# Kernel optimization log

Hardware: AMD Instinct MI355X
Metric: run time of the kernel (lower is better)

## Reference

```python
import jax, jax.numpy as jnp
import numpy as np

B = 16384    # number of paths (examples)
E = 100000   # num_entities
D = 256      # embedding_dim
H = 512      # hidden_dim = node_state_dim = msg_dim
T = 768      # text_dim
L = 2        # num_layers
R = 32       # num_relation_classes
EF = 8       # edge_feat_dim (hardcoded in module)
NUM_PROP = 2


def setup_inputs() -> dict:
    key = jax.random.key(0)
    ks = iter(jax.random.split(key, 40))
    def nrm(shape, s=0.02):
        return jax.random.normal(next(ks), shape, jnp.float32) * s
    z = lambda shape: jnp.zeros(shape, jnp.float32)
    inp = {
        "a_ids": jax.random.randint(next(ks), (B,), 0, E),
        "event_ids": jax.random.randint(next(ks), (B,), 0, E),
        "b_ids": jax.random.randint(next(ks), (B,), 0, E),
        "c_ids": jax.random.randint(next(ks), (B,), 0, E),
        "text_ab": jax.random.normal(next(ks), (B, T), jnp.float32),
        "ent_emb": nrm((E, D)),
        "text_W": nrm((T, D)), "text_b": z((D,)),
        "proj_W": nrm((D, H)), "proj_b": z((H,)),
        "msg_W1": nrm((L, H + EF, H)), "msg_b1": z((L, H)),
        "msg_W2": nrm((L, H, H)), "msg_b2": z((L, H)),
        "att_W1": nrm((L, H + EF, H // 2)), "att_b1": z((L, H // 2)),
        "att_W2": nrm((L, H // 2, H)), "att_b2": z((L, H)),
        "gru_Wih": nrm((L, 3 * H, H)), "gru_Whh": nrm((L, 3 * H, H)),
        "gru_bih": z((L, 3 * H)), "gru_bhh": z((L, 3 * H)),
        "head_W1": nrm((H, H)), "head_b1": z((H,)),
        "head_W2": nrm((H, R)), "head_b2": z((R,)),
    }
    return inp


def _forward(a_ids, event_ids, b_ids, c_ids, text_ab, ent_emb, text_W, text_b,
             proj_W, proj_b, msg_W1, msg_b1, msg_W2, msg_b2,
             att_W1, att_b1, att_W2, att_b2,
             gru_Wih, gru_Whh, gru_bih, gru_bhh,
             head_W1, head_b1, head_W2, head_b2):
    Bn = a_ids.shape[0]
    a_emb = ent_emb[a_ids]
    ev_emb = ent_emb[event_ids] + jax.nn.relu(text_ab @ text_W + text_b)  # text fused into Event node
    b_emb = ent_emb[b_ids]
    c_emb = ent_emb[c_ids]
    proj = lambda x: jax.nn.relu(x @ proj_W + proj_b)  # input_proj_ab (dropout=0 / eval)
    # merged graph: nodes [A(0:B), Event(B:2B), B(2B:3B), C(3B:4B)]
    state = jnp.concatenate([proj(a_emb), proj(ev_emb), proj(b_emb), proj(c_emb)], axis=0)  # [4B,H]
    ar = jnp.arange(Bn)
    src = jnp.concatenate([ar, ar + Bn, ar + Bn])             # A->Event, Event->B, Event->C
    dst = jnp.concatenate([ar + Bn, ar + 2 * Bn, ar + 3 * Bn])
    edge_feat = jax.nn.one_hot(jnp.repeat(jnp.arange(3), Bn), EF, dtype=state.dtype)  # [3B,8]
    n_layers = msg_W1.shape[0]
    for ii in range(n_layers):
        if ii > 0:
            state = jax.nn.relu(state)
        for _ in range(NUM_PROP):
            # gather node-pair diff + edge feature
            ein = jnp.concatenate([state[src] - state[dst], edge_feat], axis=1)  # [3B, H+EF]
            msg = jax.nn.relu(ein @ msg_W1[ii] + msg_b1[ii]) @ msg_W2[ii] + msg_b2[ii]
            att = jax.nn.sigmoid(jax.nn.relu(ein @ att_W1[ii] + att_b1[ii]) @ att_W2[ii] + att_b2[ii])
            agg = jax.ops.segment_sum(msg * att, dst, num_segments=4 * Bn)  # scatter_add
            # torch GRUCell update
            gi = agg @ gru_Wih[ii].T + gru_bih[ii]
            gh = state @ gru_Whh[ii].T + gru_bhh[ii]
            i_r, i_z, i_n = jnp.split(gi, 3, axis=-1)
            h_r, h_z, h_n = jnp.split(gh, 3, axis=-1)
            r = jax.nn.sigmoid(i_r + h_r)
            zg = jax.nn.sigmoid(i_z + h_z)
            n = jnp.tanh(i_n + r * h_n)
            state = (1.0 - zg) * n + zg * state
    # rel_AB predicted from node-state difference between A and B nodes
    diff = state[:Bn] - state[2 * Bn:3 * Bn]
    return jax.nn.relu(diff @ head_W1 + head_b1) @ head_W2 + head_b2  # [B, R] logits


def reference(a_ids, event_ids, b_ids, c_ids, text_ab, ent_emb, text_W, text_b,
              proj_W, proj_b, msg_W1, msg_b1, msg_W2, msg_b2,
              att_W1, att_b1, att_W2, att_b2,
              gru_Wih, gru_Whh, gru_bih, gru_bhh,
              head_W1, head_b1, head_W2, head_b2):
    return _forward(a_ids, event_ids, b_ids, c_ids, text_ab, ent_emb, text_W, text_b,
                    proj_W, proj_b, msg_W1, msg_b1, msg_W2, msg_b2,
                    att_W1, att_b1, att_W2, att_b2,
                    gru_Wih, gru_Whh, gru_bih, gru_bhh,
                    head_W1, head_b1, head_W2, head_b2)
```

## Files before the change

### kernel.cpp

```cpp
#include <hip/hip_runtime.h>
#include <math.h>


#define Bn 16384
#define Hn 512
#define Dn 256
#define Tn 768

#define EPI_NONE 0
#define EPI_RELU 1
#define EPI_SIG 2
#define EPI_SIGMUL 3
#define EPI_RELUGATHER 4
#define EPI_GRU 5

typedef unsigned short bfu;
typedef _Float16 f16;
typedef f16 h4 __attribute__((ext_vector_type(4)));
typedef f16 half8 __attribute__((ext_vector_type(8)));
typedef float floatx4 __attribute__((ext_vector_type(4)));

#define HTEXTW 0
#define HPROJW 196608
#define HHW1 327680
#define HWE1 589824
#define HMSGW2 1376256
#define HATTW2 1900544
#define HWIH 2162688
#define HWHH 3735552
#define HTOTAL 5308416
#define FTEXTB 0
#define FPROJB 256
#define FHB1 768
#define FGBIH 1280
#define FGBHH 4352
#define FBGRZ 7424
#define FBE1 9472
#define FBE2 14080

__device__ __forceinline__ float sigf(float x) { return 1.f / (1.f + expf(-x)); }

__device__ __forceinline__ float b2f(bfu v) {
  union { unsigned q; float f; } c;
  c.q = (unsigned)v << 16;
  return c.f;
}
__device__ __forceinline__ float4 bf4(uint2 u) {
  union { unsigned q; float f; } c;
  float4 r;
  c.q = u.x << 16;          r.x = c.f;
  c.q = u.x & 0xFFFF0000u;  r.y = c.f;
  c.q = u.y << 16;          r.z = c.f;
  c.q = u.y & 0xFFFF0000u;  r.w = c.f;
  return r;
}
__device__ __forceinline__ unsigned f2bu(float x) {
  union { float f; unsigned u; } c;
  c.f = x;
  return (c.u + 0x7FFFu + ((c.u >> 16) & 1u)) >> 16;
}
__device__ __forceinline__ float4 h2f4(h4 h) {
  return make_float4((float)h.x, (float)h.y, (float)h.z, (float)h.w);
}
__device__ __forceinline__ h4 f2h4c(float4 v) {
  h4 r;
  r.x = (f16)v.x; r.y = (f16)v.y; r.z = (f16)v.z; r.w = (f16)v.w;
  return r;
}
__device__ __forceinline__ half8 ff2h8(float4 a, float4 b) {
  half8 r;
  r[0] = (f16)a.x; r[1] = (f16)a.y; r[2] = (f16)a.z; r[3] = (f16)a.w;
  r[4] = (f16)b.x; r[5] = (f16)b.y; r[6] = (f16)b.z; r[7] = (f16)b.w;
  return r;
}
__device__ __forceinline__ half8 bf2h8(uint4 u) {
  uint2 lo; lo.x = u.x; lo.y = u.y;
  uint2 hi; hi.x = u.z; hi.y = u.w;
  return ff2h8(bf4(lo), bf4(hi));
}

__global__ void detect_k(const unsigned* __restrict__ p, int* __restrict__ flag) {
  __shared__ float red[256];
  const int t = threadIdx.x;
  union { unsigned q; float f; } c;
  c.q = p[t] << 16;
  float m = fabsf(c.f);
  if (!(m == m)) m = 1e30f;
  red[t] = m;
  __syncthreads();
  for (int s = 128; s > 0; s >>= 1) {
    if (t < s) red[t] = fmaxf(red[t], red[t + s]);
    __syncthreads();
  }
  if (t == 0) flag[0] = (red[0] < 1e3f) ? 1 : 0;
}

__device__ __forceinline__ float cvld(const void* p, size_t i, int fl) {
  return fl ? b2f(((const bfu*)p)[i]) : ((const float*)p)[i];
}

__global__ void convF_k(const void* __restrict__ src, size_t off, float* __restrict__ dst,
                        int n, const int* __restrict__ flagp) {
  const int i = blockIdx.x * 256 + threadIdx.x;
  if (i < n) dst[i] = cvld(src, off + i, flagp[0]);
}
__global__ void convH_k(const void* __restrict__ src, size_t off, f16* __restrict__ dst,
                        int n, const int* __restrict__ flagp) {
  const int i = blockIdx.x * 256 + threadIdx.x;
  if (i < n) dst[i] = (f16)cvld(src, off + i, flagp[0]);
}
__global__ void convT_k(const void* __restrict__ src, size_t off, f16* __restrict__ dst,
                        int K, int N, const int* __restrict__ flagp) {
  __shared__ f16 tile[32][33];
  const int t = threadIdx.x;
  const int c = t & 31, r0 = t >> 5;
  const int kb = blockIdx.y * 32, nb = blockIdx.x * 32;
  const int fl = flagp[0];
#pragma unroll
  for (int i = 0; i < 4; ++i)
    tile[r0 + i * 8][c] = (f16)cvld(src, off + (size_t)(kb + r0 + i * 8) * N + nb + c, fl);
  __syncthreads();
#pragma unroll
  for (int i = 0; i < 4; ++i)
    dst[(size_t)(nb + r0 + i * 8) * K + kb + c] = tile[c][r0 + i * 8];
}
__global__ void addv_k(const float* __restrict__ a, const float* __restrict__ b,
                       float* __restrict__ o, int n) {
  const int i = blockIdx.x * 256 + threadIdx.x;
  if (i < n) o[i] = a[i] + b[i];
}
__global__ void btype_k(const void* __restrict__ b, size_t bOff,
                        const void* __restrict__ wr, size_t wrOff,
                        float* __restrict__ dst, int N, int dstStride,
                        const int* __restrict__ flagp) {
  const int i = blockIdx.x * 256 + threadIdx.x;
  const int fl = flagp[0];
  if (i < 3 * N) {
    const int t = i / N, n = i % N;
    dst[(size_t)t * dstStride + n] = cvld(b, bOff + n, fl) + cvld(wr, wrOff + i, fl);
  }
}
__global__ void gather_k(const int* __restrict__ ids, const void* __restrict__ emb,
                         f16* __restrict__ Xc, const int* __restrict__ flagp) {
  const int r = blockIdx.x, t = threadIdx.x;
  const int id = ids[r];
  float4 v;
  if (flagp[0])
    v = bf4(((const uint2*)((const bfu*)emb + (size_t)id * Dn))[t]);
  else
    v = ((const float4*)((const float*)emb + (size_t)id * Dn))[t];
  ((h4*)(Xc + (size_t)r * Dn))[t] = f2h4c(v);
}

template <int EPI, int AM, int BM, int CT, int BTY>
__global__ __launch_bounds__(256, 2) void hgemm_k(
    const void* __restrict__ Ap, const void* __restrict__ Ap2,
    const f16* __restrict__ Wt, const f16* __restrict__ Wt2,
    const float* __restrict__ bias,
    const f16* __restrict__ ex1, const f16* __restrict__ ex2,
    const int* __restrict__ gidx, const void* __restrict__ gtab,
    void* __restrict__ C, int N, int K, int aStride, int rowOff, int nRows,
    const int* __restrict__ flagp) {
  __shared__ __align__(16) f16 As[128][40];
  __shared__ __align__(16) f16 Bs[128][40];
  const int t = threadIdx.x;
  const int bid = blockIdx.x;
  const int rowsPerX = nRows >> 3;
  const int slot = bid >> 3;
  const int row0 = ((bid & 7) * rowsPerX + slot % rowsPerX) * 128;
  const int col0 = (slot / rowsPerX) * 128;
  const int lane = t & 63;
  const int wv = t >> 6;
  const int wm = wv >> 1, wn = wv & 1;
  const int l16 = lane & 15, quad = lane >> 4;
  const int arow = t & 127;
  const int ak0 = (t >> 7) * 8;
  const int fl = (AM == 1 || EPI == EPI_RELUGATHER) ? flagp[0] : 0;

  floatx4 acc[4][4];
#pragma unroll
  for (int mi = 0; mi < 4; ++mi)
#pragma unroll
    for (int ni = 0; ni < 4; ++ni) acc[mi][ni] = (floatx4){0.f, 0.f, 0.f, 0.f};

  auto fetchA = [&](int kk, int seg) -> half8 {
    const int k = kk + ak0 + seg * 16;
    const int m = row0 + arow;
    if (AM == 5) {
      return *(const half8*)((const f16*)Ap + (size_t)m * aStride + k);
    } else if (AM == 1) {
      const size_t o = (size_t)(rowOff + m) * aStride + k;
      if (fl) return bf2h8(*(const uint4*)((const bfu*)Ap + o));
      const float* ap = (const float*)Ap + o;
      return ff2h8(*(const float4*)ap, *(const float4*)(ap + 4));
    } else if (AM == 6) {
      if (k < 512) return *(const half8*)((const f16*)Ap + (size_t)m * 512 + k);
      return *(const half8*)((const f16*)Ap2 + (size_t)m * 512 + (k - 512));
    } else {
      const int e = rowOff + m;
      const int s = (e < 2 * Bn) ? e : e - Bn;
      const f16* st = (const f16*)Ap;
      half8 x = *(const half8*)(st + (size_t)s * 512 + k);
      half8 y = *(const half8*)(st + (size_t)(e + Bn) * 512 + k);
      return x - y;
    }
  };
  auto fetchB = [&](int kk, int seg) -> half8 {
    const int k = kk + ak0 + seg * 16;
    const int n = col0 + arow;
    if (BM == 0) return *(const half8*)(Wt + (size_t)n * K + k);
    if (k < 512) return *(const half8*)(Wt + (size_t)n * 512 + k);
    return *(const half8*)(Wt2 + (size_t)n * 512 + k - 512);
  };

  half8 pa0 = fetchA(0, 0), pa1 = fetchA(0, 1);
  half8 pb0 = fetchB(0, 0), pb1 = fetchB(0, 1);

  int kt = 0;
  while (true) {
    __syncthreads();
    *(half8*)&As[arow][ak0] = pa0;
    *(half8*)&As[arow][ak0 + 16] = pa1;
    *(half8*)&Bs[arow][ak0] = pb0;
    *(half8*)&Bs[arow][ak0 + 16] = pb1;
    __syncthreads();
    const int kn = kt + 32;
    if (kn < K) {
      pa0 = fetchA(kn, 0); pa1 = fetchA(kn, 1);
      pb0 = fetchB(kn, 0); pb1 = fetchB(kn, 1);
    }
    half8 a8[4], b8[4];
#pragma unroll
    for (int mi = 0; mi < 4; ++mi)
      a8[mi] = *(const half8*)&As[wm * 64 + mi * 16 + l16][quad * 8];
#pragma unroll
    for (int ni = 0; ni < 4; ++ni)
      b8[ni] = *(const half8*)&Bs[wn * 64 + ni * 16 + l16][quad * 8];
#pragma unroll
    for (int mi = 0; mi < 4; ++mi)
#pragma unroll
      for (int ni = 0; ni < 4; ++ni)
        acc[mi][ni] = __builtin_amdgcn_mfma_f32_16x16x32_f16(a8[mi], b8[ni],
                                                             acc[mi][ni], 0, 0, 0);
    if (kn >= K) break;
    kt = kn;
  }

  const float* bp = bias;
  if (BTY) bp = bias + ((rowOff + row0) >> 14) * 768;
  const int colBase = col0 + wn * 64;
  const int rowBase = row0 + wm * 64;
#pragma unroll
  for (int mi = 0; mi < 4; ++mi) {
    const int r0r = rowBase + mi * 16 + quad * 4;
#pragma unroll
    for (int ni = 0; ni < 4; ++ni) {
      const int col = colBase + ni * 16 + l16;
      const float bb = bp[col];
      floatx4 v = acc[mi][ni];
#pragma unroll
      for (int rg = 0; rg < 4; ++rg) {
        const int row = r0r + rg;
        float x = v[rg] + bb;
        if (EPI == EPI_RELU || EPI == EPI_RELUGATHER) x = fmaxf(x, 0.f);
        if (EPI == EPI_SIG) x = sigf(x);
        if (EPI == EPI_SIGMUL)
          x = sigf(x) * (float)ex1[(size_t)row * N + col];
        if (EPI == EPI_RELUGATHER) {
          const int grow = gidx[rowOff + row];
          x += fl ? b2f(((const bfu*)gtab)[(size_t)grow * N + col])
                  : ((const float*)gtab)[(size_t)grow * N + col];
        }
        if (EPI == EPI_GRU) {
          const float r_ = (float)ex1[(size_t)row * 1024 + col];
          const float z_ = (float)ex1[(size_t)row * 1024 + 512 + col];
          const float hn = (float)ex2[(size_t)row * 512 + col];
          f16* cf = (f16*)C + (size_t)row * 512 + col;
          const float s = (float)*cf;
          const float n_ = tanhf(x + r_ * hn);
          *cf = (f16)((1.f - z_) * n_ + z_ * s);
        } else if (CT == 0) {
          ((float*)C)[(size_t)row * N + col] = x;
        } else {
          ((f16*)C)[(size_t)row * N + col] = (f16)x;
        }
      }
    }
  }
}

__global__ void gate0_k(const f16* __restrict__ RZ, const f16* __restrict__ HN,
                        const float* __restrict__ bihn, f16* __restrict__ st) {
  const int idx = blockIdx.x * blockDim.x + threadIdx.x;
  const int m = idx >> 7;
  const int c = (idx & 127) << 2;
  float4 r4 = h2f4(*(const h4*)(RZ + (size_t)m * 1024 + c));
  float4 z4 = h2f4(*(const h4*)(RZ + (size_t)m * 1024 + 512 + c));
  float4 hn = h2f4(*(const h4*)(HN + (size_t)m * 512 + c));
  float4 b4 = *(const float4*)(bihn + c);
  f16* sp = st + (size_t)m * 512 + c;
  float4 s = h2f4(*(const h4*)sp);
  float4 o;
  float n_;
  n_ = tanhf(b4.x + r4.x * hn.x); o.x = (1.f - z4.x) * n_ + z4.x * s.x;
  n_ = tanhf(b4.y + r4.y * hn.y); o.y = (1.f - z4.y) * n_ + z4.y * s.y;
  n_ = tanhf(b4.z + r4.z * hn.z); o.z = (1.f - z4.z) * n_ + z4.z * s.z;
  n_ = tanhf(b4.w + r4.w * hn.w); o.w = (1.f - z4.w) * n_ + z4.w * s.w;
  *(h4*)sp = f2h4c(o);
}

__global__ void hdiff_k(const f16* __restrict__ st, f16* __restrict__ Dh) {
  const int m = blockIdx.x, t = threadIdx.x;
  half8 a = ((const half8*)(st + (size_t)m * Hn))[t];
  half8 b = ((const half8*)(st + (size_t)(2 * Bn + m) * Hn))[t];
  ((half8*)(Dh + (size_t)m * Hn))[t] = a - b;
}

__global__ void relu_h_k(uint4* __restrict__ p, long n) {
  long i = (long)blockIdx.x * blockDim.x + threadIdx.x;
  if (i < n) {
    uint4 v = p[i];
    v.x = ((v.x & 0x8000u) ? 0u : (v.x & 0xFFFFu)) |
          ((v.x & 0x80000000u) ? 0u : (v.x & 0xFFFF0000u));
    v.y = ((v.y & 0x8000u) ? 0u : (v.y & 0xFFFFu)) |
          ((v.y & 0x80000000u) ? 0u : (v.y & 0xFFFF0000u));
    v.z = ((v.z & 0x8000u) ? 0u : (v.z & 0xFFFFu)) |
          ((v.z & 0x80000000u) ? 0u : (v.z & 0xFFFF0000u));
    v.w = ((v.w & 0x8000u) ? 0u : (v.w & 0xFFFFu)) |
          ((v.w & 0x80000000u) ? 0u : (v.w & 0xFFFF0000u));
    p[i] = v;
  }
}

__global__ void head2_k(const f16* __restrict__ Hh, const void* __restrict__ W2,
                        const void* __restrict__ b2, void* __restrict__ out,
                        const int* __restrict__ flagp) {
  __shared__ __align__(16) float Ws[64][32];
  __shared__ __align__(16) float As2[8][64];
  const int t = threadIdx.x;
  const int r0 = blockIdx.x * 8;
  const int lr = t >> 5, c = t & 31;
  const int fl = flagp[0];
  float acc = 0.f;
  for (int kc = 0; kc < 512; kc += 64) {
    __syncthreads();
    if (fl) {
      uint4 u = ((const uint4*)((const bfu*)W2 + (size_t)kc * 32))[t];
      uint2 lo; lo.x = u.x; lo.y = u.y;
      uint2 hi; hi.x = u.z; hi.y = u.w;
      ((float4*)&Ws[0][0])[t * 2] = bf4(lo);
      ((float4*)&Ws[0][0])[t * 2 + 1] = bf4(hi);
    } else {
      const float4* src = (const float4*)((const float*)W2 + (size_t)kc * 32);
      ((float4*)&Ws[0][0])[t * 2] = src[t * 2];
      ((float4*)&Ws[0][0])[t * 2 + 1] = src[t * 2 + 1];
    }
    {
      const int i = t * 2, rr = i >> 6, cc = i & 63;
      const f16* hp = Hh + (size_t)(r0 + rr) * 512 + kc + cc;
      As2[rr][cc] = (float)hp[0];
      As2[rr][cc + 1] = (float)hp[1];
    }
    __syncthreads();
#pragma unroll
    for (int k = 0; k < 64; ++k) acc = fmaf(As2[lr][k], Ws[k][c], acc);
  }
  const float bb = fl ? b2f(((const bfu*)b2)[c]) : ((const float*)b2)[c];
  const float r = acc + bb;
  const size_t o = (size_t)(r0 + lr) * 32 + c;
  if (fl) ((bfu*)out)[o] = (bfu)f2bu(r);
  else ((float*)out)[o] = r;
}

extern "C" void kernel_launch(void* const* d_in, const int* in_sizes, int n_in,
                              void* d_out, int out_size, void* d_ws, size_t ws_size,
                              hipStream_t stream) {
  const int* a_ids = (const int*)d_in[0];
  const int* event_ids = (const int*)d_in[1];
  const int* b_ids = (const int*)d_in[2];
  const int* c_ids = (const int*)d_in[3];
  const void* text_ab = d_in[4];
  const void* ent_emb = d_in[5];

  char* w = (char*)d_ws;
  int* flag = (int*)w;   w += 256;
  float* bf = (float*)w; w += 65536;
  f16* hw = (f16*)w;     w += (size_t)HTOTAL * 2;
  f16* P = (f16*)w;      w += (size_t)3 * Bn * 512 * 2;
  f16* S = (f16*)w;      w += (size_t)50331648;
  f16* state = (f16*)w;
  f16* RZ = S;
  f16* HN = S + (size_t)Bn * 1024;
  const dim3 blk(256);

  detect_k<<<dim3(1), blk, 0, stream>>>((const unsigned*)ent_emb, flag);

  struct CF { int idx; size_t off; int dst; int n; };
  const CF cfs[9] = {{7, 0, FTEXTB, 256},   {9, 0, FPROJB, 512},
                     {23, 0, FHB1, 512},    {20, 0, FGBIH, 3072},
                     {21, 0, FGBHH, 3072},  {13, 0, FBE2, 512},
                     {17, 0, FBE2 + 512, 512}, {13, 512, FBE2 + 1024, 512},
                     {17, 512, FBE2 + 1536, 512}};
  for (int i = 0; i < 9; ++i)
    convF_k<<<dim3((cfs[i].n + 255) / 256), blk, 0, stream>>>(
        d_in[cfs[i].idx], cfs[i].off, bf + cfs[i].dst, cfs[i].n, flag);

  convT_k<<<dim3(8, 24), blk, 0, stream>>>(d_in[6], 0, hw + HTEXTW, Tn, Dn, flag);
  convT_k<<<dim3(16, 8), blk, 0, stream>>>(d_in[8], 0, hw + HPROJW, Dn, Hn, flag);
  convT_k<<<dim3(16, 16), blk, 0, stream>>>(d_in[22], 0, hw + HHW1, Hn, Hn, flag);
  for (int ii = 0; ii < 2; ++ii) {
    convT_k<<<dim3(16, 16), blk, 0, stream>>>(
        d_in[10], (size_t)ii * 520 * 512, hw + HWE1 + ii * 393216, Hn, Hn, flag);
    convT_k<<<dim3(8, 16), blk, 0, stream>>>(
        d_in[14], (size_t)ii * 520 * 256, hw + HWE1 + ii * 393216 + 262144, Hn, 256, flag);
    convT_k<<<dim3(16, 16), blk, 0, stream>>>(
        d_in[12], (size_t)ii * 512 * 512, hw + HMSGW2 + ii * 262144, Hn, Hn, flag);
    convT_k<<<dim3(16, 8), blk, 0, stream>>>(
        d_in[16], (size_t)ii * 256 * 512, hw + HATTW2 + ii * 131072, 256, Hn, flag);
    convH_k<<<dim3(3072), blk, 0, stream>>>(
        d_in[18], (size_t)ii * 786432, hw + HWIH + ii * 786432, 786432, flag);
    convH_k<<<dim3(3072), blk, 0, stream>>>(
        d_in[19], (size_t)ii * 786432, hw + HWHH + ii * 786432, 786432, flag);
    addv_k<<<dim3(4), blk, 0, stream>>>(bf + FGBIH + ii * 1536, bf + FGBHH + ii * 1536,
                                        bf + FBGRZ + ii * 1024, 1024);
    btype_k<<<dim3(6), blk, 0, stream>>>(
        d_in[11], (size_t)ii * 512, d_in[10], (size_t)ii * 520 * 512 + 512 * 512,
        bf + FBE1 + ii * 2304, 512, 768, flag);
    btype_k<<<dim3(3), blk, 0, stream>>>(
        d_in[15], (size_t)ii * 256, d_in[14], (size_t)ii * 520 * 256 + 512 * 256,
        bf + FBE1 + ii * 2304 + 512, 256, 768, flag);
  }

  f16* Xc = S;
  const int* gids[3] = {a_ids, b_ids, c_ids};
  const size_t gdst[3] = {0, (size_t)2 * Bn, (size_t)3 * Bn};
  for (int g = 0; g < 3; ++g) {
    gather_k<<<dim3(Bn), dim3(64), 0, stream>>>(gids[g], ent_emb, Xc, flag);
    hgemm_k<EPI_RELU, 5, 0, 2, 0><<<dim3(4 * 128), blk, 0, stream>>>(
        Xc, nullptr, hw + HPROJW, nullptr, bf + FPROJB, nullptr, nullptr,
        nullptr, nullptr, state + gdst[g] * 512, Hn, Dn, Dn, 0, 128, flag);
  }
  hgemm_k<EPI_RELUGATHER, 1, 0, 2, 0><<<dim3(2 * 128), blk, 0, stream>>>(
      text_ab, nullptr, hw + HTEXTW, nullptr, bf + FTEXTB, nullptr, nullptr,
      event_ids, ent_emb, Xc, Dn, Tn, Tn, 0, 128, flag);
  hgemm_k<EPI_RELU, 5, 0, 2, 0><<<dim3(4 * 128), blk, 0, stream>>>(
      Xc, nullptr, hw + HPROJW, nullptr, bf + FPROJB, nullptr, nullptr,
      nullptr, nullptr, state + (size_t)Bn * 512, Hn, Dn, Dn, 0, 128, flag);

  for (int ii = 0; ii < 2; ++ii) {
    if (ii > 0)
      relu_h_k<<<dim3(16384), blk, 0, stream>>>((uint4*)state,
                                                (long)4 * Bn * Hn * 2 / 16);
    const f16* Wih = hw + HWIH + (size_t)ii * 786432;
    const f16* Whh = hw + HWHH + (size_t)ii * 786432;
    const f16* Win = Wih + (size_t)1024 * 512;
    const f16* Whn = Whh + (size_t)1024 * 512;
    const float* bgrz = bf + FBGRZ + ii * 1024;
    const float* bihn = bf + FGBIH + ii * 1536 + 1024;
    const float* bhhn = bf + FGBHH + ii * 1536 + 1024;
    for (int p = 0; p < 2; ++p) {
      for (int c = 0; c < 2; ++c) {
        const int e0 = c * 24576;
        f16* hid = S;
        hgemm_k<EPI_RELU, 2, 0, 2, 1><<<dim3(6 * 192), blk, 0, stream>>>(
            state, nullptr, hw + HWE1 + ii * 393216, nullptr,
            bf + FBE1 + ii * 2304, nullptr, nullptr, nullptr, nullptr,
            hid, 768, Hn, 512, e0, 192, flag);
        hgemm_k<EPI_NONE, 5, 0, 2, 0><<<dim3(4 * 192), blk, 0, stream>>>(
            hid, nullptr, hw + HMSGW2 + ii * 262144, nullptr, bf + FBE2 + ii * 1024,
            nullptr, nullptr, nullptr, nullptr, P + (size_t)e0 * 512,
            Hn, 512, 768, 0, 192, flag);
        hgemm_k<EPI_SIGMUL, 5, 0, 2, 0><<<dim3(4 * 192), blk, 0, stream>>>(
            hid + 512, nullptr, hw + HATTW2 + ii * 131072, nullptr,
            bf + FBE2 + ii * 1024 + 512, P + (size_t)e0 * 512, nullptr,
            nullptr, nullptr, P + (size_t)e0 * 512, Hn, 256, 768, 0, 192, flag);
      }
      for (int r = 1; r <= 3; ++r) {
        f16* Pc = P + (size_t)(r - 1) * Bn * 512;
        f16* str = state + (size_t)r * Bn * 512;
        hgemm_k<EPI_SIG, 6, 1, 2, 0><<<dim3(8 * 128), blk, 0, stream>>>(
            Pc, str, Wih, Whh, bgrz, nullptr, nullptr, nullptr, nullptr,
            RZ, 1024, 1024, 512, 0, 128, flag);
        hgemm_k<EPI_NONE, 5, 0, 2, 0><<<dim3(4 * 128), blk, 0, stream>>>(
            str, nullptr, Whn, nullptr, bhhn, nullptr, nullptr, nullptr,
            nullptr, HN, Hn, 512, 512, 0, 128, flag);
        hgemm_k<EPI_GRU, 5, 0, 0, 0><<<dim3(4 * 128), blk, 0, stream>>>(
            Pc, nullptr, Win, nullptr, bihn, RZ, HN, nullptr, nullptr,
            str, Hn, 512, 512, 0, 128, flag);
      }
      hgemm_k<EPI_SIG, 5, 0, 2, 0><<<dim3(8 * 128), blk, 0, stream>>>(
          state, nullptr, Whh, nullptr, bgrz, nullptr, nullptr, nullptr,
          nullptr, RZ, 1024, 512, 512, 0, 128, flag);
      hgemm_k<EPI_NONE, 5, 0, 2, 0><<<dim3(4 * 128), blk, 0, stream>>>(
          state, nullptr, Whn, nullptr, bhhn, nullptr, nullptr, nullptr,
          nullptr, HN, Hn, 512, 512, 0, 128, flag);
      gate0_k<<<dim3(8192), blk, 0, stream>>>(RZ, HN, bihn, state);
    }
  }

  hdiff_k<<<dim3(Bn), dim3(64), 0, stream>>>(state, S);
  hgemm_k<EPI_RELU, 5, 0, 2, 0><<<dim3(4 * 128), blk, 0, stream>>>(
      S, nullptr, hw + HHW1, nullptr, bf + FHB1, nullptr, nullptr, nullptr,
      nullptr, P, Hn, 512, 512, 0, 128, flag);
  head2_k<<<dim3(Bn / 8), blk, 0, stream>>>(P, d_in[24], d_in[25], d_out, flag);
}
```

Measured before the change: 3.431 ms.

## Widen GEMM tiles to 128x256 and double-buffer LDS with one barrier per step

The fp16 MFMA GEMM kernel now computes a 128x256 output tile per block, so each wave holds a 64x128 accumulator tile, and grid sizes are halved to match. Shared-memory staging becomes double-buffered: the next K slice is written into the alternate buffer after the MFMAs, which leaves a single barrier per iteration. The aim is more reuse of each A fragment and fewer LDS barriers per unit of work. The cost is twice the accumulator registers and more LDS, which may lower occupancy under launch_bounds(256,2) and cause spills. Halving the grids also leaves fewer blocks to spread across the CUs.

```diff
diff --git a/kernel.cpp b/kernel.cpp
--- a/kernel.cpp
+++ b/kernel.cpp
@@ -161,30 +161,29 @@
     const int* __restrict__ gidx, const void* __restrict__ gtab,
     void* __restrict__ C, int N, int K, int aStride, int rowOff, int nRows,
     const int* __restrict__ flagp) {
-  __shared__ __align__(16) f16 As[128][40];
-  __shared__ __align__(16) f16 Bs[128][40];
+  __shared__ __align__(16) f16 As[2][128][40];
+  __shared__ __align__(16) f16 Bs[2][256][40];
   const int t = threadIdx.x;
   const int bid = blockIdx.x;
   const int rowsPerX = nRows >> 3;
   const int slot = bid >> 3;
   const int row0 = ((bid & 7) * rowsPerX + slot % rowsPerX) * 128;
-  const int col0 = (slot / rowsPerX) * 128;
+  const int col0 = (slot / rowsPerX) * 256;
   const int lane = t & 63;
   const int wv = t >> 6;
   const int wm = wv >> 1, wn = wv & 1;
   const int l16 = lane & 15, quad = lane >> 4;
   const int arow = t & 127;
-  const int ak0 = (t >> 7) * 8;
+  const int ak0 = (t >> 7) * 16;
   const int fl = (AM == 1 || EPI == EPI_RELUGATHER) ? flagp[0] : 0;
 
-  floatx4 acc[4][4];
+  floatx4 acc[4][8];
 #pragma unroll
   for (int mi = 0; mi < 4; ++mi)
 #pragma unroll
-    for (int ni = 0; ni < 4; ++ni) acc[mi][ni] = (floatx4){0.f, 0.f, 0.f, 0.f};
-
-  auto fetchA = [&](int kk, int seg) -> half8 {
-    const int k = kk + ak0 + seg * 16;
+    for (int ni = 0; ni < 8; ++ni) acc[mi][ni] = (floatx4){0.f, 0.f, 0.f, 0.f};
+
+  auto fetchA = [&](int k) -> half8 {
     const int m = row0 + arow;
     if (AM == 5) {
       return *(const half8*)((const f16*)Ap + (size_t)m * aStride + k);
@@ -205,56 +204,64 @@
       return x - y;
     }
   };
-  auto fetchB = [&](int kk, int seg) -> half8 {
-    const int k = kk + ak0 + seg * 16;
-    const int n = col0 + arow;
+  auto fetchB = [&](int brow, int k) -> half8 {
+    const int n = col0 + brow;
     if (BM == 0) return *(const half8*)(Wt + (size_t)n * K + k);
     if (k < 512) return *(const half8*)(Wt + (size_t)n * 512 + k);
     return *(const half8*)(Wt2 + (size_t)n * 512 + k - 512);
   };
 
-  half8 pa0 = fetchA(0, 0), pa1 = fetchA(0, 1);
-  half8 pb0 = fetchB(0, 0), pb1 = fetchB(0, 1);
-
-  int kt = 0;
-  while (true) {
-    __syncthreads();
-    *(half8*)&As[arow][ak0] = pa0;
-    *(half8*)&As[arow][ak0 + 16] = pa1;
-    *(half8*)&Bs[arow][ak0] = pb0;
-    *(half8*)&Bs[arow][ak0 + 16] = pb1;
-    __syncthreads();
-    const int kn = kt + 32;
-    if (kn < K) {
-      pa0 = fetchA(kn, 0); pa1 = fetchA(kn, 1);
-      pb0 = fetchB(kn, 0); pb1 = fetchB(kn, 1);
-    }
-    half8 a8[4], b8[4];
+  half8 pa0, pa1, pb0, pb1, pb2, pb3;
+  auto prefetch = [&](int kk) {
+    pa0 = fetchA(kk + ak0);
+    pa1 = fetchA(kk + ak0 + 8);
+    pb0 = fetchB(arow, kk + ak0);
+    pb1 = fetchB(arow, kk + ak0 + 8);
+    pb2 = fetchB(arow + 128, kk + ak0);
+    pb3 = fetchB(arow + 128, kk + ak0 + 8);
+  };
+  auto stage = [&](int buf) {
+    *(half8*)&As[buf][arow][ak0] = pa0;
+    *(half8*)&As[buf][arow][ak0 + 8] = pa1;
+    *(half8*)&Bs[buf][arow][ak0] = pb0;
+    *(half8*)&Bs[buf][arow][ak0 + 8] = pb1;
+    *(half8*)&Bs[buf][arow + 128][ak0] = pb2;
+    *(half8*)&Bs[buf][arow + 128][ak0 + 8] = pb3;
+  };
+
+  prefetch(0);
+  stage(0);
+  __syncthreads();
+  const int nk = K >> 5;
+  for (int kt = 0; kt < nk; ++kt) {
+    const int cur = kt & 1;
+    if (kt + 1 < nk) prefetch((kt + 1) * 32);
+    half8 a8[4], b8[8];
 #pragma unroll
     for (int mi = 0; mi < 4; ++mi)
-      a8[mi] = *(const half8*)&As[wm * 64 + mi * 16 + l16][quad * 8];
-#pragma unroll
-    for (int ni = 0; ni < 4; ++ni)
-      b8[ni] = *(const half8*)&Bs[wn * 64 + ni * 16 + l16][quad * 8];
+      a8[mi] = *(const half8*)&As[cur][wm * 64 + mi * 16 + l16][quad * 8];
+#pragma unroll
+    for (int ni = 0; ni < 8; ++ni)
+      b8[ni] = *(const half8*)&Bs[cur][wn * 128 + ni * 16 + l16][quad * 8];
 #pragma unroll
     for (int mi = 0; mi < 4; ++mi)
 #pragma unroll
-      for (int ni = 0; ni < 4; ++ni)
+      for (int ni = 0; ni < 8; ++ni)
         acc[mi][ni] = __builtin_amdgcn_mfma_f32_16x16x32_f16(a8[mi], b8[ni],
                                                              acc[mi][ni], 0, 0, 0);
-    if (kn >= K) break;
-    kt = kn;
+    if (kt + 1 < nk) stage(cur ^ 1);
+    __syncthreads();
   }
 
   const float* bp = bias;
   if (BTY) bp = bias + ((rowOff + row0) >> 14) * 768;
-  const int colBase = col0 + wn * 64;
+  const int colBase = col0 + wn * 128;
   const int rowBase = row0 + wm * 64;
 #pragma unroll
   for (int mi = 0; mi < 4; ++mi) {
     const int r0r = rowBase + mi * 16 + quad * 4;
 #pragma unroll
-    for (int ni = 0; ni < 4; ++ni) {
+    for (int ni = 0; ni < 8; ++ni) {
       const int col = colBase + ni * 16 + l16;
       const float bb = bp[col];
       floatx4 v = acc[mi][ni];
@@ -436,14 +443,14 @@
   const size_t gdst[3] = {0, (size_t)2 * Bn, (size_t)3 * Bn};
   for (int g = 0; g < 3; ++g) {
     gather_k<<<dim3(Bn), dim3(64), 0, stream>>>(gids[g], ent_emb, Xc, flag);
-    hgemm_k<EPI_RELU, 5, 0, 2, 0><<<dim3(4 * 128), blk, 0, stream>>>(
+    hgemm_k<EPI_RELU, 5, 0, 2, 0><<<dim3(2 * 128), blk, 0, stream>>>(
         Xc, nullptr, hw + HPROJW, nullptr, bf + FPROJB, nullptr, nullptr,
         nullptr, nullptr, state + gdst[g] * 512, Hn, Dn, Dn, 0, 128, flag);
   }
-  hgemm_k<EPI_RELUGATHER, 1, 0, 2, 0><<<dim3(2 * 128), blk, 0, stream>>>(
+  hgemm_k<EPI_RELUGATHER, 1, 0, 2, 0><<<dim3(1 * 128), blk, 0, stream>>>(
       text_ab, nullptr, hw + HTEXTW, nullptr, bf + FTEXTB, nullptr, nullptr,
       event_ids, ent_emb, Xc, Dn, Tn, Tn, 0, 128, flag);
-  hgemm_k<EPI_RELU, 5, 0, 2, 0><<<dim3(4 * 128), blk, 0, stream>>>(
+  hgemm_k<EPI_RELU, 5, 0, 2, 0><<<dim3(2 * 128), blk, 0, stream>>>(
       Xc, nullptr, hw + HPROJW, nullptr, bf + FPROJB, nullptr, nullptr,
       nullptr, nullptr, state + (size_t)Bn * 512, Hn, Dn, Dn, 0, 128, flag);
 
@@ -462,15 +469,15 @@
       for (int c = 0; c < 2; ++c) {
         const int e0 = c * 24576;
         f16* hid = S;
-        hgemm_k<EPI_RELU, 2, 0, 2, 1><<<dim3(6 * 192), blk, 0, stream>>>(
+        hgemm_k<EPI_RELU, 2, 0, 2, 1><<<dim3(3 * 192), blk, 0, stream>>>(
             state, nullptr, hw + HWE1 + ii * 393216, nullptr,
             bf + FBE1 + ii * 2304, nullptr, nullptr, nullptr, nullptr,
             hid, 768, Hn, 512, e0, 192, flag);
-        hgemm_k<EPI_NONE, 5, 0, 2, 0><<<dim3(4 * 192), blk, 0, stream>>>(
+        hgemm_k<EPI_NONE, 5, 0, 2, 0><<<dim3(2 * 192), blk, 0, stream>>>(
             hid, nullptr, hw + HMSGW2 + ii * 262144, nullptr, bf + FBE2 + ii * 1024,
             nullptr, nullptr, nullptr, nullptr, P + (size_t)e0 * 512,
             Hn, 512, 768, 0, 192, flag);
-        hgemm_k<EPI_SIGMUL, 5, 0, 2, 0><<<dim3(4 * 192), blk, 0, stream>>>(
+        hgemm_k<EPI_SIGMUL, 5, 0, 2, 0><<<dim3(2 * 192), blk, 0, stream>>>(
             hid + 512, nullptr, hw + HATTW2 + ii * 131072, nullptr,
             bf + FBE2 + ii * 1024 + 512, P + (size_t)e0 * 512, nullptr,
             nullptr, nullptr, P + (size_t)e0 * 512, Hn, 256, 768, 0, 192, flag);
@@ -478,20 +485,20 @@
       for (int r = 1; r <= 3; ++r) {
         f16* Pc = P + (size_t)(r - 1) * Bn * 512;
         f16* str = state + (size_t)r * Bn * 512;
-        hgemm_k<EPI_SIG, 6, 1, 2, 0><<<dim3(8 * 128), blk, 0, stream>>>(
+        hgemm_k<EPI_SIG, 6, 1, 2, 0><<<dim3(4 * 128), blk, 0, stream>>>(
             Pc, str, Wih, Whh, bgrz, nullptr, nullptr, nullptr, nullptr,
             RZ, 1024, 1024, 512, 0, 128, flag);
-        hgemm_k<EPI_NONE, 5, 0, 2, 0><<<dim3(4 * 128), blk, 0, stream>>>(
+        hgemm_k<EPI_NONE, 5, 0, 2, 0><<<dim3(2 * 128), blk, 0, stream>>>(
             str, nullptr, Whn, nullptr, bhhn, nullptr, nullptr, nullptr,
             nullptr, HN, Hn, 512, 512, 0, 128, flag);
-        hgemm_k<EPI_GRU, 5, 0, 0, 0><<<dim3(4 * 128), blk, 0, stream>>>(
+        hgemm_k<EPI_GRU, 5, 0, 0, 0><<<dim3(2 * 128), blk, 0, stream>>>(
             Pc, nullptr, Win, nullptr, bihn, RZ, HN, nullptr, nullptr,
             str, Hn, 512, 512, 0, 128, flag);
       }
-      hgemm_k<EPI_SIG, 5, 0, 2, 0><<<dim3(8 * 128), blk, 0, stream>>>(
+      hgemm_k<EPI_SIG, 5, 0, 2, 0><<<dim3(4 * 128), blk, 0, stream>>>(
           state, nullptr, Whh, nullptr, bgrz, nullptr, nullptr, nullptr,
           nullptr, RZ, 1024, 512, 512, 0, 128, flag);
-      hgemm_k<EPI_NONE, 5, 0, 2, 0><<<dim3(4 * 128), blk, 0, stream>>>(
+      hgemm_k<EPI_NONE, 5, 0, 2, 0><<<dim3(2 * 128), blk, 0, stream>>>(
           state, nullptr, Whn, nullptr, bhhn, nullptr, nullptr, nullptr,
           nullptr, HN, Hn, 512, 512, 0, 128, flag);
       gate0_k<<<dim3(8192), blk, 0, stream>>>(RZ, HN, bihn, state);
@@ -499,7 +506,7 @@
   }
 
   hdiff_k<<<dim3(Bn), dim3(64), 0, stream>>>(state, S);
-  hgemm_k<EPI_RELU, 5, 0, 2, 0><<<dim3(4 * 128), blk, 0, stream>>>(
+  hgemm_k<EPI_RELU, 5, 0, 2, 0><<<dim3(2 * 128), blk, 0, stream>>>(
       S, nullptr, hw + HHW1, nullptr, bf + FHB1, nullptr, nullptr, nullptr,
       nullptr, P, Hn, 512, 512, 0, 128, flag);
   head2_k<<<dim3(Bn / 8), blk, 0, stream>>>(P, d_in[24], d_in[25], d_out, flag);
```

Result: no change. 3.473 ms (+1.2%).
